# Performance work log

Measured on AMD Instinct MI355X. Metric: run time of the kernel, lower is better.

The kernel has to match this reference:

```python
import jax, jax.numpy as jnp
import numpy as np

N_CELLS = 50000
N_GENES = 2000
HIDDEN = 128
HEADS = 4
HEAD_DIM = HIDDEN // HEADS
E_FULL = 800000
E_PRUNED = 400000
LN_EPS = 1e-6
NEG_SLOPE = 0.2


def setup_inputs() -> dict:
    key = jax.random.key(0)
    ks = jax.random.split(key, 20)
    s_in = 1.0 / np.sqrt(N_GENES)
    s_h = 1.0 / np.sqrt(HIDDEN)
    inp = {
        "node_features": jax.random.normal(ks[0], (N_CELLS, N_GENES), jnp.float32),
        "full_edge_index": jax.random.randint(ks[1], (2, E_FULL), 0, N_CELLS, jnp.int64 if jax.config.jax_enable_x64 else jnp.int32),
        "full_edge_weights": jax.random.uniform(ks[2], (E_FULL, 1), jnp.float32),
        "pruned_edge_index": jax.random.randint(ks[3], (2, E_PRUNED), 0, N_CELLS, jnp.int64 if jax.config.jax_enable_x64 else jnp.int32),
        "pruned_edge_weights": jax.random.uniform(ks[4], (E_PRUNED, 1), jnp.float32),
        "alpha": jax.random.uniform(ks[5], (), jnp.float32),
        # input projection
        "ip_w": jax.random.normal(ks[6], (N_GENES, HIDDEN), jnp.float32) * s_in,
        "ip_b": jnp.zeros((HIDDEN,), jnp.float32),
        # GAT full graph
        "gf_wsrc": jax.random.normal(ks[7], (HIDDEN, HIDDEN), jnp.float32) * s_h,
        "gf_wdst": jax.random.normal(ks[8], (HIDDEN, HIDDEN), jnp.float32) * s_h,
        "gf_wedge": jax.random.normal(ks[9], (1, HIDDEN), jnp.float32),
        "gf_attn": jax.random.normal(ks[10], (HEADS, HEAD_DIM), jnp.float32) * (1.0 / np.sqrt(HEAD_DIM)),
        "gf_bias": jnp.zeros((HIDDEN,), jnp.float32),
        # GAT pruned graph
        "gp_wsrc": jax.random.normal(ks[11], (HIDDEN, HIDDEN), jnp.float32) * s_h,
        "gp_wdst": jax.random.normal(ks[12], (HIDDEN, HIDDEN), jnp.float32) * s_h,
        "gp_wedge": jax.random.normal(ks[13], (1, HIDDEN), jnp.float32),
        "gp_attn": jax.random.normal(ks[14], (HEADS, HEAD_DIM), jnp.float32) * (1.0 / np.sqrt(HEAD_DIM)),
        "gp_bias": jnp.zeros((HIDDEN,), jnp.float32),
        # LayerNorm
        "ln_scale": jnp.ones((HIDDEN,), jnp.float32),
        "ln_bias": jnp.zeros((HIDDEN,), jnp.float32),
    }
    return inp


def _gatv2(h, edge_index, edge_w, wsrc, wdst, wedge, attn, bias):
    """GATv2 with edge features: e_ij = a_h . leaky_relu(Ws h_i + Wd h_j + We w_ij),
    segment-softmax over destination nodes, scatter-aggregate Ws h_src, concat heads."""
    n = h.shape[0]
    src, dst = edge_index[0], edge_index[1]
    hs = (h @ wsrc).reshape(n, HEADS, HEAD_DIM)
    hd = (h @ wdst).reshape(n, HEADS, HEAD_DIM)
    ew = (edge_w @ wedge).reshape(-1, HEADS, HEAD_DIM)  # [E,H,D]
    z = jax.nn.leaky_relu(hs[src] + hd[dst] + ew, NEG_SLOPE)  # [E,H,D]
    logits = jnp.einsum('ehd,hd->eh', z, attn)  # [E,H]
    # segment softmax over incoming edges of each dst node
    m = jax.ops.segment_max(logits, dst, num_segments=n)
    m = jnp.where(jnp.isfinite(m), m, 0.0)
    ex = jnp.exp(logits - m[dst])
    denom = jax.ops.segment_sum(ex, dst, num_segments=n)
    att = ex / (denom[dst] + 1e-16)  # [E,H]
    out = jax.ops.segment_sum(att[..., None] * hs[src], dst, num_segments=n)  # [n,H,D]
    return out.reshape(n, HIDDEN) + bias


def _layer_norm(x, scale, bias):
    mu = jnp.mean(x, axis=-1, keepdims=True)
    var = jnp.mean(jnp.square(x - mu), axis=-1, keepdims=True)
    return (x - mu) * jax.lax.rsqrt(var + LN_EPS) * scale + bias


def reference(node_features, full_edge_index, full_edge_weights, pruned_edge_index,
              pruned_edge_weights, alpha, ip_w, ip_b,
              gf_wsrc, gf_wdst, gf_wedge, gf_attn, gf_bias,
              gp_wsrc, gp_wdst, gp_wedge, gp_attn, gp_bias,
              ln_scale, ln_bias):
    h = node_features @ ip_w + ip_b  # [n, hidden]
    h_full = _gatv2(h, full_edge_index, full_edge_weights, gf_wsrc, gf_wdst, gf_wedge, gf_attn, gf_bias)
    h_pruned = _gatv2(h, pruned_edge_index, pruned_edge_weights, gp_wsrc, gp_wdst, gp_wedge, gp_attn, gp_bias)
    h = (1.0 - alpha) * h_full + alpha * h_pruned
    h = jax.nn.elu(h)
    return _layer_norm(h, ln_scale, ln_bias)
```

## Files before the change

kernel.cpp:

```cpp
#include <hip/hip_runtime.h>
#include <hip/hip_bf16.h>

#define N_GENES 2000
#define SA 72
#define SH 136

typedef __attribute__((ext_vector_type(8))) short frag8;
typedef __attribute__((ext_vector_type(4))) float facc4;

static __device__ __forceinline__ unsigned short f2bf(float f) {
    unsigned int u = __float_as_uint(f);
    unsigned int r = (u + 0x7FFFu + ((u >> 16) & 1u)) >> 16;
    return (unsigned short)r;
}
static __device__ __forceinline__ ushort2 pk2(float a, float b) {
    __hip_bfloat162 r = __float22bfloat162_rn(float2{a, b});
    return *(ushort2*)&r;
}

__global__ void prep(const float* __restrict__ ip_w,
                     const float* __restrict__ ws_f, const float* __restrict__ wd_f,
                     const float* __restrict__ ws_p, const float* __restrict__ wd_p,
                     unsigned short* __restrict__ Bt1,
                     unsigned short* __restrict__ Bf, unsigned short* __restrict__ Bp,
                     int* __restrict__ deg, unsigned int* __restrict__ counter, int n2) {
    int idx = blockIdx.x * blockDim.x + threadIdx.x;
    if (idx < n2) deg[idx] = 0;
    if (idx == 0) counter[0] = 0u;
    if (idx < 128 * 2048) {
        int nrow = idx >> 11, k = idx & 2047;
        unsigned short v = 0;
        if (k < N_GENES) v = f2bf(ip_w[(size_t)k * 128 + nrow]);
        Bt1[idx] = v;
    } else {
        int q = idx - 128 * 2048;
        if (q >= 2 * 256 * 128) return;
        int g = q >> 15;
        int r = (q >> 7) & 255;
        int k = q & 127;
        const float* w = (g == 0) ? (r < 128 ? ws_f : wd_f) : (r < 128 ? ws_p : wd_p);
        (g == 0 ? Bf : Bp)[(r << 7) | k] = f2bf(w[k * 128 + (r & 127)]);
    }
}

__global__ __launch_bounds__(256) void gemm_deg(const float* __restrict__ A,
                                                const unsigned short* __restrict__ Bt,
                                                const float* __restrict__ bias,
                                                const unsigned short* __restrict__ Bf,
                                                const unsigned short* __restrict__ Bp,
                                                unsigned short* __restrict__ Cf,
                                                unsigned short* __restrict__ Cp,
                                                int M, int K, int gemmBlocks,
                                                const int* __restrict__ dst_f, int Ef,
                                                const int* __restrict__ dst_p, int Ep,
                                                int* __restrict__ deg, int N) {
    if (blockIdx.x >= gemmBlocks) {
        int e = (blockIdx.x - gemmBlocks) * 256 + threadIdx.x;
        if (e < Ef) atomicAdd(&deg[dst_f[e]], 1);
        else if (e < Ef + Ep) atomicAdd(&deg[N + dst_p[e - Ef]], 1);
        return;
    }
    const int Kpad = 2048;
    __shared__ __align__(16) unsigned short lA[64 * SA];
    __shared__ __align__(16) unsigned short lH[64 * SH];
    int t = threadIdx.x, lane = t & 63, wv = t >> 6;
    int lr = lane & 15, lq = lane >> 4;
    facc4 acc[4][2];
#pragma unroll
    for (int i = 0; i < 4; i++)
#pragma unroll
        for (int j = 0; j < 2; j++) acc[i][j] = (facc4){0.f, 0.f, 0.f, 0.f};
    int row_base = blockIdx.x * 64;

    int ar_r[4], ar_c[4];
    const float* ar_p[4];
#pragma unroll
    for (int j = 0; j < 4; j++) {
        int q = j * 256 + t;
        ar_r[j] = q >> 4;
        ar_c[j] = (q & 15) * 4;
        int rg = row_base + ar_r[j];
        if (rg >= M) rg = M - 1;
        ar_p[j] = A + (size_t)rg * K + ar_c[j];
    }
    const unsigned short* bp[4];
#pragma unroll
    for (int ks = 0; ks < 2; ks++)
#pragma unroll
        for (int ni = 0; ni < 2; ni++) {
            int col = wv * 32 + ni * 16 + lr;
            bp[ks * 2 + ni] = Bt + (size_t)col * Kpad + ks * 32 + lq * 8;
        }

    float4 ar[4];
    frag8 bfr[4];
#pragma unroll
    for (int j = 0; j < 4; j++) ar[j] = *(const float4*)(ar_p[j]);
#pragma unroll
    for (int f = 0; f < 4; f++) bfr[f] = *(const frag8*)(bp[f]);

    for (int k0 = 0; k0 < Kpad; k0 += 64) {
        __syncthreads();
#pragma unroll
        for (int j = 0; j < 4; j++) {
            ushort2 u01 = pk2(ar[j].x, ar[j].y);
            ushort2 u23 = pk2(ar[j].z, ar[j].w);
            ushort4 u = {u01.x, u01.y, u23.x, u23.y};
            *(ushort4*)&lA[ar_r[j] * SA + ar_c[j]] = u;
        }
        __syncthreads();
        int kn = k0 + 64;
        frag8 bfn[4];
        if (kn < Kpad) {
#pragma unroll
            for (int j = 0; j < 4; j++) {
                int kk = kn + ar_c[j];
                float4 v = {0.f, 0.f, 0.f, 0.f};
                if (kk < K) v = *(const float4*)(ar_p[j] + kn);
                ar[j] = v;
            }
#pragma unroll
            for (int f = 0; f < 4; f++) bfn[f] = *(const frag8*)(bp[f] + kn);
        }
#pragma unroll
        for (int ks = 0; ks < 2; ks++) {
            frag8 af[4];
#pragma unroll
            for (int mi = 0; mi < 4; mi++)
                af[mi] = *(const frag8*)&lA[(mi * 16 + lr) * SA + ks * 32 + lq * 8];
#pragma unroll
            for (int mi = 0; mi < 4; mi++)
#pragma unroll
                for (int ni = 0; ni < 2; ni++)
                    acc[mi][ni] = __builtin_amdgcn_mfma_f32_16x16x32_bf16(af[mi], bfr[ks * 2 + ni], acc[mi][ni], 0, 0, 0);
        }
        if (kn < Kpad) {
#pragma unroll
            for (int f = 0; f < 4; f++) bfr[f] = bfn[f];
        }
    }
    __syncthreads();
#pragma unroll
    for (int mi = 0; mi < 4; mi++) {
#pragma unroll
        for (int r = 0; r < 4; r++) {
            int row = mi * 16 + lq * 4 + r;
#pragma unroll
            for (int ni = 0; ni < 2; ni++) {
                int col = wv * 32 + ni * 16 + lr;
                lH[row * SH + col] = f2bf(acc[mi][ni][r] + bias[col]);
            }
        }
    }
    __syncthreads();
#pragma unroll 1
    for (int g = 0; g < 2; g++) {
        const unsigned short* B2 = g ? Bp : Bf;
        unsigned short* Cb = g ? Cp : Cf;
        facc4 a2[4][4];
#pragma unroll
        for (int i = 0; i < 4; i++)
#pragma unroll
            for (int j = 0; j < 4; j++) a2[i][j] = (facc4){0.f, 0.f, 0.f, 0.f};
#pragma unroll
        for (int ks = 0; ks < 4; ks++) {
            frag8 af[4], bf[4];
#pragma unroll
            for (int mi = 0; mi < 4; mi++)
                af[mi] = *(const frag8*)&lH[(mi * 16 + lr) * SH + ks * 32 + lq * 8];
#pragma unroll
            for (int ni = 0; ni < 4; ni++)
                bf[ni] = *(const frag8*)(B2 + ((wv * 64 + ni * 16 + lr) << 7) + ks * 32 + lq * 8);
#pragma unroll
            for (int mi = 0; mi < 4; mi++)
#pragma unroll
                for (int ni = 0; ni < 4; ni++)
                    a2[mi][ni] = __builtin_amdgcn_mfma_f32_16x16x32_bf16(af[mi], bf[ni], a2[mi][ni], 0, 0, 0);
        }
#pragma unroll
        for (int mi = 0; mi < 4; mi++) {
#pragma unroll
            for (int r = 0; r < 4; r++) {
                int row = row_base + mi * 16 + lq * 4 + r;
                if (row < M) {
#pragma unroll
                    for (int ni = 0; ni < 4; ni++) {
                        int col = wv * 64 + ni * 16 + lr;
                        Cb[(size_t)row * 256 + col] = f2bf(a2[mi][ni][r]);
                    }
                }
            }
        }
    }
}

__global__ __launch_bounds__(256) void seg_assign(const int* __restrict__ deg,
                                                  int* __restrict__ offs,
                                                  int* __restrict__ cur,
                                                  unsigned int* __restrict__ counter, int n2) {
    int i = blockIdx.x * 256 + threadIdx.x;
    int lane = threadIdx.x & 63;
    int c = (i < n2) ? deg[i] : 0;
    int incl = c;
#pragma unroll
    for (int o = 1; o < 64; o <<= 1) {
        int y = __shfl_up(incl, o);
        if (lane >= o) incl += y;
    }
    int wtot = __shfl(incl, 63);
    int base = 0;
    if (lane == 63) base = (int)atomicAdd(counter, (unsigned int)wtot);
    base = __shfl(base, 63);
    int start = base + incl - c;
    if (i < n2) { offs[i] = start; cur[i] = start; }
}

__global__ void fill2(const int* __restrict__ src_f, const int* __restrict__ dst_f,
                      const float* __restrict__ ew_f, int Ef,
                      const int* __restrict__ src_p, const int* __restrict__ dst_p,
                      const float* __restrict__ ew_p, int Ep,
                      int* __restrict__ cur, int2* __restrict__ srcw, int N) {
    int e = blockIdx.x * blockDim.x + threadIdx.x;
    if (e >= Ef + Ep) return;
    int g = (e >= Ef);
    int ee = g ? e - Ef : e;
    int d = g ? dst_p[ee] : dst_f[ee];
    int node = g ? N + d : d;
    int p = atomicAdd(&cur[node], 1);
    int s = g ? src_p[ee] : src_f[ee];
    float w = g ? ew_p[ee] : ew_f[ee];
    srcw[p] = make_int2(s, __float_as_int(w));
}

__global__ __launch_bounds__(256) void gat2(const int* __restrict__ offs,
                                            const int* __restrict__ deg,
                                            const int2* __restrict__ srcw,
                                            const unsigned short* __restrict__ hshd_f,
                                            const unsigned short* __restrict__ hshd_p,
                                            const float* __restrict__ wedge_f,
                                            const float* __restrict__ attn_f,
                                            const float* __restrict__ bias_f,
                                            const float* __restrict__ wedge_p,
                                            const float* __restrict__ attn_p,
                                            const float* __restrict__ bias_p,
                                            float* __restrict__ out_full,
                                            float* __restrict__ out_pruned, int N) {
    int node = blockIdx.x * 4 + (threadIdx.x >> 6);
    if (node >= 2 * N) return;
    int g = node >= N;
    int onode = g ? node - N : node;
    const unsigned short* hshd = g ? hshd_p : hshd_f;
    const float* wedge = g ? wedge_p : wedge_f;
    const float* attn = g ? attn_p : attn_f;
    const float* bias = g ? bias_p : bias_f;
    float* out = g ? out_pruned : out_full;
    int lane = threadIdx.x & 63;
    int d2 = lane * 2;
    const float LOG2E = 1.4426950408889634f;
    const float2 wv = *(const float2*)&wedge[d2];
    float2 av = *(const float2*)&attn[d2];
    av.x *= LOG2E; av.y *= LOG2E;
    unsigned int hdraw = *(const unsigned int*)&hshd[(size_t)onode * 256 + 128 + d2];
    const float hd0 = __uint_as_float(hdraw << 16);
    const float hd1 = __uint_as_float(hdraw & 0xffff0000u);
    int s = offs[node], cnt = deg[node];
    float m = -INFINITY, l = 0.f, acc0 = 0.f, acc1 = 0.f;
    if (cnt > 0) {
        int last = s + cnt - 1;
        auto CL = [last](int j) { return j > last ? last : j; };
        int2 e0 = srcw[s], e1 = srcw[CL(s + 1)], e2 = srcw[CL(s + 2)], e3 = srcw[CL(s + 3)];
        int2 e4 = srcw[CL(s + 4)], e5 = srcw[CL(s + 5)];
        unsigned int hr0 = *(const unsigned int*)&hshd[(size_t)e0.x * 256 + d2];
        unsigned int hr1 = *(const unsigned int*)&hshd[(size_t)e1.x * 256 + d2];
        unsigned int hr2 = *(const unsigned int*)&hshd[(size_t)e2.x * 256 + d2];
        unsigned int hr3 = *(const unsigned int*)&hshd[(size_t)e3.x * 256 + d2];
        for (int i = 0; i < cnt; i += 2) {
            int2 ea = srcw[CL(s + i + 6)], eb = srcw[CL(s + i + 7)];
            unsigned int hr4 = *(const unsigned int*)&hshd[(size_t)e4.x * 256 + d2];
            unsigned int hr5 = *(const unsigned int*)&hshd[(size_t)e5.x * 256 + d2];
            {
                float h0 = __uint_as_float(hr0 << 16);
                float h1 = __uint_as_float(hr0 & 0xffff0000u);
                float w = __int_as_float(e0.y);
                float z0 = fmaf(w, wv.x, h0 + hd0); z0 = (z0 > 0.f) ? z0 : 0.2f * z0;
                float z1 = fmaf(w, wv.y, h1 + hd1); z1 = (z1 > 0.f) ? z1 : 0.2f * z1;
                float t = z0 * av.x + z1 * av.y;
                t += __shfl_xor(t, 1);
                t += __shfl_xor(t, 2);
                t += __shfl_xor(t, 4);
                t += __shfl_xor(t, 8);
                float mn = fmaxf(m, t);
                float sc = __builtin_amdgcn_exp2f(m - mn);
                float p = __builtin_amdgcn_exp2f(t - mn);
                l = l * sc + p;
                acc0 = acc0 * sc + p * h0;
                acc1 = acc1 * sc + p * h1;
                m = mn;
            }
            if (i + 1 < cnt) {
                float h0 = __uint_as_float(hr1 << 16);
                float h1 = __uint_as_float(hr1 & 0xffff0000u);
                float w = __int_as_float(e1.y);
                float z0 = fmaf(w, wv.x, h0 + hd0); z0 = (z0 > 0.f) ? z0 : 0.2f * z0;
                float z1 = fmaf(w, wv.y, h1 + hd1); z1 = (z1 > 0.f) ? z1 : 0.2f * z1;
                float t = z0 * av.x + z1 * av.y;
                t += __shfl_xor(t, 1);
                t += __shfl_xor(t, 2);
                t += __shfl_xor(t, 4);
                t += __shfl_xor(t, 8);
                float mn = fmaxf(m, t);
                float sc = __builtin_amdgcn_exp2f(m - mn);
                float p = __builtin_amdgcn_exp2f(t - mn);
                l = l * sc + p;
                acc0 = acc0 * sc + p * h0;
                acc1 = acc1 * sc + p * h1;
                m = mn;
            }
            e0 = e2; e1 = e3; e2 = e4; e3 = e5; e4 = ea; e5 = eb;
            hr0 = hr2; hr1 = hr3; hr2 = hr4; hr3 = hr5;
        }
    }
    float inv = 1.f / (l + 1e-16f);
    const float2 bv = *(const float2*)&bias[d2];
    float2 o;
    o.x = acc0 * inv + bv.x;
    o.y = acc1 * inv + bv.y;
    *(float2*)&out[(size_t)onode * 128 + d2] = o;
}

__global__ __launch_bounds__(256) void final_kernel(const float* __restrict__ hf,
                                                    float* __restrict__ out,
                                                    const float* __restrict__ alpha_p,
                                                    const float* __restrict__ scale,
                                                    const float* __restrict__ beta, int n) {
    int node = blockIdx.x * 4 + (threadIdx.x >> 6);
    if (node >= n) return;
    int lane = threadIdx.x & 63;
    int d2 = lane * 2;
    float a = *alpha_p;
    float2 f = *(const float2*)&hf[(size_t)node * 128 + d2];
    float2 p = *(const float2*)&out[(size_t)node * 128 + d2];
    float x0 = (1.f - a) * f.x + a * p.x;
    float x1 = (1.f - a) * f.y + a * p.y;
    x0 = (x0 > 0.f) ? x0 : expm1f(x0);
    x1 = (x1 > 0.f) ? x1 : expm1f(x1);
    float sm = x0 + x1;
#pragma unroll
    for (int o = 32; o >= 1; o >>= 1) sm += __shfl_xor(sm, o);
    float mu = sm * (1.f / 128.f);
    float d0 = x0 - mu, d1 = x1 - mu;
    float v = d0 * d0 + d1 * d1;
#pragma unroll
    for (int o = 32; o >= 1; o >>= 1) v += __shfl_xor(v, o);
    float rstd = rsqrtf(v * (1.f / 128.f) + 1e-6f);
    const float2 sv = *(const float2*)&scale[d2];
    const float2 bv = *(const float2*)&beta[d2];
    float2 o2;
    o2.x = d0 * rstd * sv.x + bv.x;
    o2.y = d1 * rstd * sv.y + bv.y;
    *(float2*)&out[(size_t)node * 128 + d2] = o2;
}

extern "C" void kernel_launch(void* const* d_in, const int* in_sizes, int n_in,
                              void* d_out, int out_size, void* d_ws, size_t ws_size,
                              hipStream_t stream) {
    const float* nf = (const float*)d_in[0];
    const int* fei = (const int*)d_in[1];
    const float* few = (const float*)d_in[2];
    const int* pei = (const int*)d_in[3];
    const float* pew = (const float*)d_in[4];
    const float* alpha = (const float*)d_in[5];
    const float* ip_w = (const float*)d_in[6];
    const float* ip_b = (const float*)d_in[7];
    const float* gf_wsrc = (const float*)d_in[8];
    const float* gf_wdst = (const float*)d_in[9];
    const float* gf_wedge = (const float*)d_in[10];
    const float* gf_attn = (const float*)d_in[11];
    const float* gf_bias = (const float*)d_in[12];
    const float* gp_wsrc = (const float*)d_in[13];
    const float* gp_wdst = (const float*)d_in[14];
    const float* gp_wedge = (const float*)d_in[15];
    const float* gp_attn = (const float*)d_in[16];
    const float* gp_bias = (const float*)d_in[17];
    const float* ln_scale = (const float*)d_in[18];
    const float* ln_bias = (const float*)d_in[19];

    const int N = in_sizes[0] / N_GENES;
    const int Ef = in_sizes[1] / 2;
    const int Ep = in_sizes[3] / 2;
    const int Etot = Ef + Ep;
    const int n2 = 2 * N;

    char* base = (char*)d_ws;
    size_t off = 0;
    auto carve = [&](size_t bytes) -> char* {
        char* p = base + off;
        off = (off + bytes + 255) & ~(size_t)255;
        return p;
    };
    unsigned short* Bt1 = (unsigned short*)carve((size_t)128 * 2048 * 2);
    unsigned short* Bf = (unsigned short*)carve(256 * 128 * 2);
    unsigned short* Bp = (unsigned short*)carve(256 * 128 * 2);
    unsigned short* hshd_f = (unsigned short*)carve((size_t)N * 256 * 2);
    unsigned short* hshd_p = (unsigned short*)carve((size_t)N * 256 * 2);
    float* h_full = (float*)carve((size_t)N * 128 * 4);
    int* deg = (int*)carve((size_t)n2 * 4);
    int* offs = (int*)carve((size_t)n2 * 4);
    int* cur = (int*)carve((size_t)n2 * 4);
    unsigned int* counter = (unsigned int*)carve(4);
    int2* srcw = (int2*)carve((size_t)Etot * 8);
    float* out_f = (float*)d_out;

    const int* src_f = fei;
    const int* dst_f = fei + Ef;
    const int* src_p = pei;
    const int* dst_p = pei + Ep;

    prep<<<(128 * 2048 + 2 * 256 * 128 + 255) / 256, 256, 0, stream>>>(
        ip_w, gf_wsrc, gf_wdst, gp_wsrc, gp_wdst, Bt1, Bf, Bp, deg, counter, n2);

    int gb1 = (N + 63) / 64;
    int degb = (Etot + 255) / 256;
    gemm_deg<<<gb1 + degb, 256, 0, stream>>>(nf, Bt1, ip_b, Bf, Bp, hshd_f, hshd_p,
                                             N, N_GENES, gb1,
                                             dst_f, Ef, dst_p, Ep, deg, N);

    seg_assign<<<(n2 + 255) / 256, 256, 0, stream>>>(deg, offs, cur, counter, n2);

    fill2<<<(Etot + 255) / 256, 256, 0, stream>>>(src_f, dst_f, few, Ef, src_p, dst_p, pew, Ep,
                                                  cur, srcw, N);

    gat2<<<(n2 + 3) / 4, 256, 0, stream>>>(offs, deg, srcw, hshd_f, hshd_p,
                                           gf_wedge, gf_attn, gf_bias,
                                           gp_wedge, gp_attn, gp_bias,
                                           h_full, out_f, N);

    final_kernel<<<(N + 3) / 4, 256, 0, stream>>>(h_full, out_f, alpha, ln_scale, ln_bias, N);
    (void)ws_size; (void)n_in; (void)out_size;
}
```

Before: 823.7 us.

## Process two destination nodes per wavefront in GAT aggregation with wider loads

```diff
diff --git a/kernel.cpp b/kernel.cpp
--- a/kernel.cpp
+++ b/kernel.cpp
@@ -198,8 +198,10 @@
                                                   int* __restrict__ offs,
                                                   int* __restrict__ cur,
                                                   unsigned int* __restrict__ counter, int n2) {
-    int i = blockIdx.x * 256 + threadIdx.x;
-    int lane = threadIdx.x & 63;
+    __shared__ int wbase[4];
+    int t = threadIdx.x;
+    int i = blockIdx.x * 256 + t;
+    int lane = t & 63, wv = t >> 6;
     int c = (i < n2) ? deg[i] : 0;
     int incl = c;
 #pragma unroll
@@ -207,11 +209,18 @@
         int y = __shfl_up(incl, o);
         if (lane >= o) incl += y;
     }
-    int wtot = __shfl(incl, 63);
-    int base = 0;
-    if (lane == 63) base = (int)atomicAdd(counter, (unsigned int)wtot);
-    base = __shfl(base, 63);
-    int start = base + incl - c;
+    if (lane == 63) wbase[wv] = incl;
+    __syncthreads();
+    if (t == 0) {
+        int s0 = wbase[0], s1 = wbase[1], s2 = wbase[2], s3 = wbase[3];
+        int b = (int)atomicAdd(counter, (unsigned int)(s0 + s1 + s2 + s3));
+        wbase[0] = b;
+        wbase[1] = b + s0;
+        wbase[2] = b + s0 + s1;
+        wbase[3] = b + s0 + s1 + s2;
+    }
+    __syncthreads();
+    int start = wbase[wv] + incl - c;
     if (i < n2) { offs[i] = start; cur[i] = start; }
 }
 
@@ -245,8 +254,12 @@
                                             const float* __restrict__ bias_p,
                                             float* __restrict__ out_full,
                                             float* __restrict__ out_pruned, int N) {
-    int node = blockIdx.x * 4 + (threadIdx.x >> 6);
-    if (node >= 2 * N) return;
+    int wid = blockIdx.x * 4 + (threadIdx.x >> 6);
+    if (wid * 2 >= 2 * N) return;
+    int lane = threadIdx.x & 63;
+    int half = lane >> 5;
+    int wl = lane & 31;
+    int node = wid * 2 + half;
     int g = node >= N;
     int onode = g ? node - N : node;
     const unsigned short* hshd = g ? hshd_p : hshd_f;
@@ -254,66 +267,82 @@
     const float* attn = g ? attn_p : attn_f;
     const float* bias = g ? bias_p : bias_f;
     float* out = g ? out_pruned : out_full;
-    int lane = threadIdx.x & 63;
-    int d2 = lane * 2;
+    int d4 = wl * 4;
     const float LOG2E = 1.4426950408889634f;
-    const float2 wv = *(const float2*)&wedge[d2];
-    float2 av = *(const float2*)&attn[d2];
-    av.x *= LOG2E; av.y *= LOG2E;
-    unsigned int hdraw = *(const unsigned int*)&hshd[(size_t)onode * 256 + 128 + d2];
-    const float hd0 = __uint_as_float(hdraw << 16);
-    const float hd1 = __uint_as_float(hdraw & 0xffff0000u);
+    float4 wv4 = *(const float4*)&wedge[d4];
+    float4 av4 = *(const float4*)&attn[d4];
+    av4.x *= LOG2E; av4.y *= LOG2E; av4.z *= LOG2E; av4.w *= LOG2E;
+    uint2 hdr = *(const uint2*)&hshd[(size_t)onode * 256 + 128 + d4];
+    const float hd0 = __uint_as_float(hdr.x << 16);
+    const float hd1 = __uint_as_float(hdr.x & 0xffff0000u);
+    const float hd2 = __uint_as_float(hdr.y << 16);
+    const float hd3 = __uint_as_float(hdr.y & 0xffff0000u);
     int s = offs[node], cnt = deg[node];
-    float m = -INFINITY, l = 0.f, acc0 = 0.f, acc1 = 0.f;
-    if (cnt > 0) {
-        int last = s + cnt - 1;
+    if (cnt <= 0) s = 0;
+    int mc = max(cnt, __shfl_xor(cnt, 32));
+    float m = -INFINITY, l = 0.f;
+    float a0 = 0.f, a1 = 0.f, a2 = 0.f, a3 = 0.f;
+    if (mc > 0) {
+        int last = s + (cnt > 0 ? cnt : 1) - 1;
         auto CL = [last](int j) { return j > last ? last : j; };
-        int2 e0 = srcw[s], e1 = srcw[CL(s + 1)], e2 = srcw[CL(s + 2)], e3 = srcw[CL(s + 3)];
+        int2 e0 = srcw[CL(s)], e1 = srcw[CL(s + 1)], e2 = srcw[CL(s + 2)], e3 = srcw[CL(s + 3)];
         int2 e4 = srcw[CL(s + 4)], e5 = srcw[CL(s + 5)];
-        unsigned int hr0 = *(const unsigned int*)&hshd[(size_t)e0.x * 256 + d2];
-        unsigned int hr1 = *(const unsigned int*)&hshd[(size_t)e1.x * 256 + d2];
-        unsigned int hr2 = *(const unsigned int*)&hshd[(size_t)e2.x * 256 + d2];
-        unsigned int hr3 = *(const unsigned int*)&hshd[(size_t)e3.x * 256 + d2];
-        for (int i = 0; i < cnt; i += 2) {
+        uint2 hr0 = *(const uint2*)&hshd[(size_t)e0.x * 256 + d4];
+        uint2 hr1 = *(const uint2*)&hshd[(size_t)e1.x * 256 + d4];
+        uint2 hr2 = *(const uint2*)&hshd[(size_t)e2.x * 256 + d4];
+        uint2 hr3 = *(const uint2*)&hshd[(size_t)e3.x * 256 + d4];
+        for (int i = 0; i < mc; i += 2) {
             int2 ea = srcw[CL(s + i + 6)], eb = srcw[CL(s + i + 7)];
-            unsigned int hr4 = *(const unsigned int*)&hshd[(size_t)e4.x * 256 + d2];
-            unsigned int hr5 = *(const unsigned int*)&hshd[(size_t)e5.x * 256 + d2];
+            uint2 hr4 = *(const uint2*)&hshd[(size_t)e4.x * 256 + d4];
+            uint2 hr5 = *(const uint2*)&hshd[(size_t)e5.x * 256 + d4];
             {
-                float h0 = __uint_as_float(hr0 << 16);
-                float h1 = __uint_as_float(hr0 & 0xffff0000u);
+                float h0 = __uint_as_float(hr0.x << 16);
+                float h1 = __uint_as_float(hr0.x & 0xffff0000u);
+                float h2 = __uint_as_float(hr0.y << 16);
+                float h3 = __uint_as_float(hr0.y & 0xffff0000u);
                 float w = __int_as_float(e0.y);
-                float z0 = fmaf(w, wv.x, h0 + hd0); z0 = (z0 > 0.f) ? z0 : 0.2f * z0;
-                float z1 = fmaf(w, wv.y, h1 + hd1); z1 = (z1 > 0.f) ? z1 : 0.2f * z1;
-                float t = z0 * av.x + z1 * av.y;
+                float z0 = fmaf(w, wv4.x, h0 + hd0); z0 = (z0 > 0.f) ? z0 : 0.2f * z0;
+                float z1 = fmaf(w, wv4.y, h1 + hd1); z1 = (z1 > 0.f) ? z1 : 0.2f * z1;
+                float z2 = fmaf(w, wv4.z, h2 + hd2); z2 = (z2 > 0.f) ? z2 : 0.2f * z2;
+                float z3 = fmaf(w, wv4.w, h3 + hd3); z3 = (z3 > 0.f) ? z3 : 0.2f * z3;
+                float t = fmaf(z3, av4.w, fmaf(z2, av4.z, fmaf(z1, av4.y, z0 * av4.x)));
                 t += __shfl_xor(t, 1);
                 t += __shfl_xor(t, 2);
                 t += __shfl_xor(t, 4);
-                t += __shfl_xor(t, 8);
                 float mn = fmaxf(m, t);
                 float sc = __builtin_amdgcn_exp2f(m - mn);
                 float p = __builtin_amdgcn_exp2f(t - mn);
+                p = (i < cnt) ? p : 0.f;
                 l = l * sc + p;
-                acc0 = acc0 * sc + p * h0;
-                acc1 = acc1 * sc + p * h1;
+                a0 = fmaf(p, h0, a0 * sc);
+                a1 = fmaf(p, h1, a1 * sc);
+                a2 = fmaf(p, h2, a2 * sc);
+                a3 = fmaf(p, h3, a3 * sc);
                 m = mn;
             }
-            if (i + 1 < cnt) {
-                float h0 = __uint_as_float(hr1 << 16);
-                float h1 = __uint_as_float(hr1 & 0xffff0000u);
+            {
+                float h0 = __uint_as_float(hr1.x << 16);
+                float h1 = __uint_as_float(hr1.x & 0xffff0000u);
+                float h2 = __uint_as_float(hr1.y << 16);
+                float h3 = __uint_as_float(hr1.y & 0xffff0000u);
                 float w = __int_as_float(e1.y);
-                float z0 = fmaf(w, wv.x, h0 + hd0); z0 = (z0 > 0.f) ? z0 : 0.2f * z0;
-                float z1 = fmaf(w, wv.y, h1 + hd1); z1 = (z1 > 0.f) ? z1 : 0.2f * z1;
-                float t = z0 * av.x + z1 * av.y;
+                float z0 = fmaf(w, wv4.x, h0 + hd0); z0 = (z0 > 0.f) ? z0 : 0.2f * z0;
+                float z1 = fmaf(w, wv4.y, h1 + hd1); z1 = (z1 > 0.f) ? z1 : 0.2f * z1;
+                float z2 = fmaf(w, wv4.z, h2 + hd2); z2 = (z2 > 0.f) ? z2 : 0.2f * z2;
+                float z3 = fmaf(w, wv4.w, h3 + hd3); z3 = (z3 > 0.f) ? z3 : 0.2f * z3;
+                float t = fmaf(z3, av4.w, fmaf(z2, av4.z, fmaf(z1, av4.y, z0 * av4.x)));
                 t += __shfl_xor(t, 1);
                 t += __shfl_xor(t, 2);
                 t += __shfl_xor(t, 4);
-                t += __shfl_xor(t, 8);
                 float mn = fmaxf(m, t);
                 float sc = __builtin_amdgcn_exp2f(m - mn);
                 float p = __builtin_amdgcn_exp2f(t - mn);
+                p = (i + 1 < cnt) ? p : 0.f;
                 l = l * sc + p;
-                acc0 = acc0 * sc + p * h0;
-                acc1 = acc1 * sc + p * h1;
+                a0 = fmaf(p, h0, a0 * sc);
+                a1 = fmaf(p, h1, a1 * sc);
+                a2 = fmaf(p, h2, a2 * sc);
+                a3 = fmaf(p, h3, a3 * sc);
                 m = mn;
             }
             e0 = e2; e1 = e3; e2 = e4; e3 = e5; e4 = ea; e5 = eb;
@@ -321,11 +350,13 @@
         }
     }
     float inv = 1.f / (l + 1e-16f);
-    const float2 bv = *(const float2*)&bias[d2];
-    float2 o;
-    o.x = acc0 * inv + bv.x;
-    o.y = acc1 * inv + bv.y;
-    *(float2*)&out[(size_t)onode * 128 + d2] = o;
+    const float4 bv = *(const float4*)&bias[d4];
+    float4 o;
+    o.x = fmaf(a0, inv, bv.x);
+    o.y = fmaf(a1, inv, bv.y);
+    o.z = fmaf(a2, inv, bv.z);
+    o.w = fmaf(a3, inv, bv.w);
+    *(float4*)&out[(size_t)onode * 128 + d4] = o;
 }
 
 __global__ __launch_bounds__(256) void final_kernel(const float* __restrict__ hf,
@@ -430,10 +461,11 @@
     fill2<<<(Etot + 255) / 256, 256, 0, stream>>>(src_f, dst_f, few, Ef, src_p, dst_p, pew, Ep,
                                                   cur, srcw, N);
 
-    gat2<<<(n2 + 3) / 4, 256, 0, stream>>>(offs, deg, srcw, hshd_f, hshd_p,
-                                           gf_wedge, gf_attn, gf_bias,
-                                           gp_wedge, gp_attn, gp_bias,
-                                           h_full, out_f, N);
+    int gwaves = (n2 + 1) / 2;
+    gat2<<<(gwaves + 3) / 4, 256, 0, stream>>>(offs, deg, srcw, hshd_f, hshd_p,
+                                               gf_wedge, gf_attn, gf_bias,
+                                               gp_wedge, gp_attn, gp_bias,
+                                               h_full, out_f, N);
 
     final_kernel<<<(N + 3) / 4, 256, 0, stream>>>(h_full, out_f, alpha, ln_scale, ln_bias, N);
     (void)ws_size; (void)n_in; (void)out_size;
```

Result: faster. 802.1 us (-2.6%).
